# Kernel optimization log

Hardware: AMD Instinct MI355X
Metric: run time of the kernel (lower is better)

Reference implementation:

```python
import jax, jax.numpy as jnp
import numpy as np

# ---- problem constants (the torch module's `params` dict) ----
D = H = W = 128          # volume_shape
HS = WS = 128            # slice_shape
N_SLICES = 16
PSF = 3                  # PSF kernel is PSF^3 taps
K = PSF ** 3
RES_RATIO = 1.5          # res_s / res_r: slice pixel spacing in volume-voxel units
N_ITER = 10              # CG iterations (tol = 0.0 -> fixed trip count)
PSF_SIGMA = 0.8


def _corners(pts):
    """8-corner trilinear indices/weights with zero contribution out of bounds.
    pts: [..., 3] in (x, y, z) voxel coords. Returns (list of int32 linear idx, list of weights).
    Gather and scatter share this so A and At are exact transposes (required for CG)."""
    x, y, z = pts[..., 0], pts[..., 1], pts[..., 2]
    x0f, y0f, z0f = jnp.floor(x), jnp.floor(y), jnp.floor(z)
    fx, fy, fz = x - x0f, y - y0f, z - z0f
    x0, y0, z0 = x0f.astype(jnp.int32), y0f.astype(jnp.int32), z0f.astype(jnp.int32)
    idxs, ws = [], []
    for dz in (0, 1):
        for dy in (0, 1):
            for dx in (0, 1):
                xi, yi, zi = x0 + dx, y0 + dy, z0 + dz
                w = (fx if dx else 1.0 - fx) * (fy if dy else 1.0 - fy) * (fz if dz else 1.0 - fz)
                inb = (xi >= 0) & (xi < W) & (yi >= 0) & (yi < H) & (zi >= 0) & (zi < D)
                idxs.append(jnp.where(inb, (zi * H + yi) * W + xi, 0))
                ws.append(jnp.where(inb, w, 0.0))
    return idxs, ws


def _sample_points(transforms):
    """PSF sample points of every slice pixel mapped into volume voxel coords.
    transforms: [N, 3, 4] rigid (R | t). Returns [N, HS, WS, K, 3] in (x, y, z)."""
    u = (jnp.arange(WS, dtype=jnp.float32) - (WS - 1) / 2) * RES_RATIO
    v = (jnp.arange(HS, dtype=jnp.float32) - (HS - 1) / 2) * RES_RATIO
    base = jnp.stack(jnp.broadcast_arrays(u[None, :], v[:, None], jnp.zeros((HS, WS), jnp.float32)), -1)  # [HS,WS,3]
    ax = jnp.arange(PSF, dtype=jnp.float32) - (PSF - 1) / 2
    oz, oy, ox = jnp.meshgrid(ax, ax, ax, indexing='ij')
    offs = jnp.stack([ox.ravel(), oy.ravel(), oz.ravel()], -1)            # [K,3] voxel units
    pts = base[:, :, None, :] + offs[None, None, :, :]                     # [HS,WS,K,3] in slice frame
    R, t = transforms[:, :3, :3], transforms[:, :3, 3]
    pts = jnp.einsum('hwkc,nrc->nhwkr', pts, R) + t[:, None, None, None, :]
    center = jnp.array([(W - 1) / 2, (H - 1) / 2, (D - 1) / 2], jnp.float32)
    return pts + center


def A_op(transforms, vol, psf_flat):
    """slice_acquisition: PSF-weighted trilinear gather from volume -> slices [N,1,HS,WS]."""
    pts = _sample_points(transforms)
    flat = vol.reshape(-1)
    idxs, ws = _corners(pts)
    vals = sum(w * flat[i] for i, w in zip(idxs, ws))                      # [N,HS,WS,K]
    return jnp.einsum('nhwk,k->nhw', vals, psf_flat)[:, None]


def At_op(transforms, slices, psf_flat):
    """slice_acquisition_adjoint: PSF-weighted trilinear scatter-add of slices -> volume."""
    pts = _sample_points(transforms)
    wv = slices[:, 0, :, :, None] * psf_flat                               # [N,HS,WS,K]
    idxs, ws = _corners(pts)
    flat = jnp.zeros(D * H * W, slices.dtype)
    for i, w in zip(idxs, ws):
        flat = flat.at[i.reshape(-1)].add((w * wv).reshape(-1))
    return flat.reshape(1, 1, D, H, W)


def _dot(a, b):
    return jnp.vdot(a.reshape(-1), b.reshape(-1))


def cg_solve(AtA, b, x0, n_iter):
    r0 = b - AtA(x0)
    def body(state, _):
        x, r, p, rr = state
        Ap = AtA(p)
        alpha = rr / _dot(p, Ap)
        x = x + alpha * p
        r = r - alpha * Ap
        rr_new = _dot(r, r)
        p = r + (rr_new / rr) * p
        return (x, r, p, rr_new), None
    (x, _, _, _), _ = jax.lax.scan(body, (x0, r0, r0, _dot(r0, r0)), None, length=n_iter)
    return x


def _rigid_transforms(n, rng):
    # small random rotations (Rodrigues) + z-stacked translations, like motion-corrupted slice stacks
    ang = rng.uniform(-0.1, 0.1, (n, 3)).astype(np.float32)
    mats = []
    for a in ang:
        th = float(np.linalg.norm(a)) + 1e-8
        k = a / th
        Kx = np.array([[0, -k[2], k[1]], [k[2], 0, -k[0]], [-k[1], k[0], 0]], np.float32)
        mats.append(np.eye(3, dtype=np.float32) + np.sin(th) * Kx + (1 - np.cos(th)) * (Kx @ Kx))
    R = np.stack(mats)
    t = np.zeros((n, 3), np.float32)
    t[:, 2] = (np.arange(n) - (n - 1) / 2) * RES_RATIO
    t[:, :2] = rng.uniform(-2.0, 2.0, (n, 2)).astype(np.float32)
    return jnp.asarray(np.concatenate([R, t[:, :, None]], axis=-1))        # [n,3,4]


def setup_inputs() -> dict:
    key = jax.random.key(0)
    k1, k2 = jax.random.split(key)
    rng = np.random.default_rng(0)
    theta = _rigid_transforms(N_SLICES, rng)
    slices = jax.random.uniform(k1, (N_SLICES, 1, HS, WS), jnp.float32)
    volume = jax.random.uniform(k2, (1, 1, D, H, W), jnp.float32)
    ax = np.arange(PSF) - (PSF - 1) / 2
    zz, yy, xx = np.meshgrid(ax, ax, ax, indexing='ij')
    psf = np.exp(-(xx ** 2 + yy ** 2 + zz ** 2) / (2 * PSF_SIGMA ** 2)).astype(np.float32)
    psf /= psf.sum()
    return {"theta": theta, "slices": slices, "volume": volume, "psf": jnp.asarray(psf)}


def reference(theta, slices, volume, psf):
    psf_flat = psf.reshape(-1)
    AtA = lambda v: At_op(theta, A_op(theta, v, psf_flat), psf_flat)
    b = At_op(theta, slices, psf_flat)          # b = At(y); p is None, mu = 0
    x = cg_solve(AtA, b, volume, N_ITER)
    return jax.nn.relu(x)                       # output_relu=True
```

## Files before the change

### kernel.cpp

```cpp
#include <hip/hip_runtime.h>
#include <math.h>

constexpr int VOX = 128 * 128 * 128;
constexpr int NPIX = 16 * 128 * 128;
constexpr int NS = 16;
constexpr float RES_RATIO = 1.5f;
constexpr int CSTR = 128;
constexpr int TNX = 19, TNY = 19, TNZ = 10;


__global__ __launch_bounds__(512) void prep_kernel(
    const float* __restrict__ theta, const float* __restrict__ psf,
    float* __restrict__ cst, int* __restrict__ zb)
{
    int tid = threadIdx.x;
    int n = tid >> 5, j = tid & 31;
    if (n < NS) {
        const float* T = theta + n * 12;
        float* C = cst + n * CSTR;
        if (j < 12) C[j] = T[j];
        if (j == 12) {
            float r00=T[0], r01=T[1], r02=T[2],  t0=T[3];
            float r10=T[4], r11=T[5], r12=T[6],  t1=T[7];
            float r20=T[8], r21=T[9], r22=T[10], t2=T[11];
            float tc0 = t0 + 63.5f, tc1 = t1 + 63.5f, tc2 = t2 + 63.5f;
            C[12]=tc0; C[13]=tc1; C[14]=tc2;
            float C2 = fabsf(r02)+fabsf(r12)+fabsf(r22);
            C[15] = fabsf(r00)+fabsf(r10)+fabsf(r20);
            C[16] = fabsf(r01)+fabsf(r11)+fabsf(r21);
            C[17] = C2;
            C[18] = fabsf(r00)+fabsf(r01)+fabsf(r02);
            C[19] = fabsf(r10)+fabsf(r11)+fabsf(r12);
            C[20] = fabsf(r20)+fabsf(r21)+fabsf(r22);
            float mx = fmaxf(tc0, 127.0f - tc0);
            float my = fmaxf(tc1, 127.0f - tc1);
            float marg = 1.05f + C2 + fabsf(r02)*mx + fabsf(r12)*my;
            float inv = 1.0f / fabsf(r22);
            C[21] = tc2 - marg * inv;
            C[22] = tc2 + marg * inv;
        }
        if (j < 27) {
            float ox = (float)(j % 3) - 1.0f;
            float oy = (float)((j / 3) % 3) - 1.0f;
            float oz = (float)(j / 9) - 1.0f;
            C[24 + 3*j + 0] = T[0]*ox + T[1]*oy + T[2]*oz;
            C[24 + 3*j + 1] = T[4]*ox + T[5]*oy + T[6]*oz;
            C[24 + 3*j + 2] = T[8]*ox + T[9]*oy + T[10]*oz;
        }
    }
    __syncthreads();
    if (tid == 0) {
        float zmin = 1e30f, zmax = -1e30f;
        for (int s = 0; s < NS; ++s) {
            zmin = fminf(zmin, cst[s * CSTR + 21]);
            zmax = fmaxf(zmax, cst[s * CSTR + 22]);
        }
        zb[0] = max(0, (int)floorf(zmin));
        zb[1] = min(127, (int)ceilf(zmax));
        float* G = cst + NS * CSTR;
        float c = psf[13];
        float ic2 = 1.0f / (c * c);
        G[0]=psf[12]; G[1]=psf[13]; G[2]=psf[14];
        G[3]=psf[10]; G[4]=psf[13]; G[5]=psf[16];
        G[6]=psf[4]*ic2; G[7]=psf[13]*ic2; G[8]=psf[22]*ic2;
    }
}

__device__ __forceinline__ void block_reduce_spread(double s, double* slots)
{
    #pragma unroll
    for (int off = 32; off > 0; off >>= 1)
        s += __shfl_down(s, off, 64);
    __shared__ double ls[4];
    if ((threadIdx.x & 63) == 0) ls[threadIdx.x >> 6] = s;
    __syncthreads();
    if (threadIdx.x == 0)
        atomicAdd(&slots[(blockIdx.x & 63) * 32], ls[0] + ls[1] + ls[2] + ls[3]);
}

__device__ __forceinline__ void block_reduce3(
    double s0, double s1, double s2, double* a0, double* a1, double* a2)
{
    #pragma unroll
    for (int off = 32; off > 0; off >>= 1) {
        s0 += __shfl_down(s0, off, 64);
        s1 += __shfl_down(s1, off, 64);
        s2 += __shfl_down(s2, off, 64);
    }
    __shared__ double ls3[12];
    int wid = threadIdx.x >> 6;
    if ((threadIdx.x & 63) == 0) {
        ls3[wid*3+0] = s0; ls3[wid*3+1] = s1; ls3[wid*3+2] = s2;
    }
    __syncthreads();
    if (threadIdx.x == 0) {
        int sl = (blockIdx.x & 63) * 32;
        atomicAdd(&a0[sl], ls3[0]+ls3[3]+ls3[6]+ls3[9]);
        atomicAdd(&a1[sl], ls3[1]+ls3[4]+ls3[7]+ls3[10]);
        atomicAdd(&a2[sl], ls3[2]+ls3[5]+ls3[8]+ls3[11]);
    }
}

__global__ __launch_bounds__(64) void a_kernel(
    const float* __restrict__ cst, const float* __restrict__ vol,
    const float* __restrict__ psf, float* __restrict__ out,
    const float* __restrict__ subsrc,
    double* __restrict__ z1, double* __restrict__ z2, double* __restrict__ z3)
{
    int tid = threadIdx.x;
    if (blockIdx.x == 0) {
        for (int i = tid; i < 2048; i += 64) {
            if (z1) z1[i] = 0.0;
            if (z2) z2[i] = 0.0;
            if (z3) z3[i] = 0.0;
        }
    }

    int b = blockIdx.x;
    int n = b >> 8;
    int pb = b & 255;
    int w0 = (pb & 15) << 3, h0 = (pb >> 4) << 3;
    int w = w0 + (tid & 7), h = h0 + (tid >> 3);
    int oidx = (n << 14) + (h << 7) + w;
    float base = subsrc ? subsrc[oidx] : 0.0f;
    float sgn = subsrc ? -1.0f : 1.0f;

    const float* C = cst + n * CSTR;
    float r00=C[0], r01=C[1];
    float r10=C[4], r11=C[5];
    float r20=C[8], r21=C[9];

    float uc = (w0 + 3.5f - 63.5f) * RES_RATIO;
    float vc = (h0 + 3.5f - 63.5f) * RES_RATIO;
    const float du = 5.25f, dv = 5.25f;
    float cx = r00*uc + r01*vc + C[12];
    float cy = r10*uc + r11*vc + C[13];
    float cz = r20*uc + r21*vc + C[14];
    float hx = fabsf(r00)*du + fabsf(r01)*dv + C[18];
    float hy = fabsf(r10)*du + fabsf(r11)*dv + C[19];
    float hz = fabsf(r20)*du + fabsf(r21)*dv + C[20];
    int tx0 = (int)floorf(cx - hx);
    int ty0 = (int)floorf(cy - hy);
    int tz0 = (int)floorf(cz - hz);

    if (tx0 >= 128 || tx0 + TNX <= 0 || ty0 >= 128 || ty0 + TNY <= 0 ||
        tz0 >= 128 || tz0 + TNZ <= 0) {
        out[oidx] = base;
        return;
    }

    __shared__ float tile[TNZ * TNY * TNX];
    for (int i = tid; i < TNZ * TNY * TNX; i += 64) {
        int xx = i % TNX; int rem = i / TNX;
        int yy = rem % TNY; int zz = rem / TNY;
        int gx = tx0 + xx, gy = ty0 + yy, gz = tz0 + zz;
        bool ok = ((unsigned)gx < 128u) & ((unsigned)gy < 128u) & ((unsigned)gz < 128u);
        int off = ok ? ((gz << 14) + (gy << 7) + gx) : 0;
        float v = vol[off];
        tile[i] = ok ? v : 0.0f;
    }
    __syncthreads();

    float u = (w - 63.5f) * RES_RATIO;
    float v = (h - 63.5f) * RES_RATIO;
    float px = fmaf(r00, u, fmaf(r01, v, C[12])) - (float)tx0;
    float py = fmaf(r10, u, fmaf(r11, v, C[13])) - (float)ty0;
    float pz = fmaf(r20, u, fmaf(r21, v, C[14])) - (float)tz0;

    const float* O = C + 24;
    float acc = 0.0f;
    for (int k = 0; k < 27; ++k) {
        float sx = px + O[3*k+0];
        float sy = py + O[3*k+1];
        float sz = pz + O[3*k+2];
        int x0 = (int)sx, y0 = (int)sy, z0 = (int)sz;
        float fx = sx - (float)x0, fy = sy - (float)y0, fz = sz - (float)z0;
        const float* tp = tile + (z0 * TNY + y0) * TNX + x0;
        float c000 = tp[0],             c001 = tp[1];
        float c010 = tp[TNX],           c011 = tp[TNX+1];
        float c100 = tp[TNY*TNX],       c101 = tp[TNY*TNX+1];
        float c110 = tp[TNY*TNX+TNX],   c111 = tp[TNY*TNX+TNX+1];
        float c00 = fmaf(fx, c001 - c000, c000);
        float c01 = fmaf(fx, c011 - c010, c010);
        float c10 = fmaf(fx, c101 - c100, c100);
        float c11 = fmaf(fx, c111 - c110, c110);
        float c0  = fmaf(fy, c01 - c00, c00);
        float c1  = fmaf(fy, c11 - c10, c10);
        acc = fmaf(psf[k], fmaf(fz, c1 - c0, c0), acc);
    }
    out[oidx] = fmaf(sgn, acc, base);
}

__global__ __launch_bounds__(256) void at_scatter_kernel(
    const float* __restrict__ cst, const float* __restrict__ sl,
    float* __restrict__ outvol)
{
    int id = blockIdx.x * 256 + threadIdx.x;
    int x = id & 127, y = (id >> 7) & 127, n = id >> 14;
    const float* C = cst + n * CSTR;
    float r00=C[0], r01=C[1], r02=C[2];
    float r10=C[4], r11=C[5], r12=C[6];
    float r20=C[8], r21=C[9], r22=C[10];
    float tc2 = C[14];
    float C0=C[15], C1=C[16], C2=C[17];

    float gx = (float)x - C[12];
    float gy = (float)y - C[13];

    float az = r02*gx + r12*gy - r22*tc2;
    float lim = 1.0f + C2 + 0.01f;
    float inv22 = 1.0f / r22;
    int z0 = (int)ceilf((-lim - az) * inv22);
    int z1v = (int)floorf(( lim - az) * inv22);
    z0 = max(z0, 0); z1v = min(z1v, 127);
    if (z0 > z1v) return;

    float ax = r00*gx + r10*gy - r20*tc2;
    float ay = r01*gx + r11*gy - r21*tc2;

    float gpxa = fmaf(r20, (float)z0, ax), gpxb = fmaf(r20, (float)z1v, ax);
    float gpya = fmaf(r21, (float)z0, ay), gpyb = fmaf(r21, (float)z1v, ay);
    int m2a = (int)floorf(2.0f*(gpxa + 95.25f - C0)) + 601;
    int m2b = (int)floorf(2.0f*(gpxb + 95.25f - C0)) + 601;
    int n2a = (int)floorf(2.0f*(gpya + 95.25f - C1)) + 601;
    int n2b = (int)floorf(2.0f*(gpyb + 95.25f - C1)) + 601;
    int wb0 = min(m2a, m2b) / 3;
    int hb0 = min(n2a, n2b) / 3;

    const float* slice_n = sl + (n << 14);
    float s[4][4];
    #pragma unroll
    for (int aa = 0; aa < 4; ++aa) {
        int hv = hb0 - 200 + aa;
        bool hok = ((unsigned)hv < 128u);
        #pragma unroll
        for (int cc = 0; cc < 4; ++cc) {
            int wv = wb0 - 200 + cc;
            bool ok = hok & ((unsigned)wv < 128u);
            int off = ok ? ((hv << 7) + wv) : 0;
            float vs = slice_n[off];
            s[aa][cc] = ok ? vs : 0.0f;
        }
    }

    const float* G = cst + NS * CSTR;
    float pfx0=G[0], pfx1=G[1], pfx2=G[2];
    float pfy0=G[3], pfy1=G[4], pfy2=G[5];
    float pfz0=G[6], pfz1=G[7], pfz2=G[8];

    int yx = (y << 7) + x;

    for (int z = z0; z <= z1v; ++z) {
        float fzv = (float)z;
        float gpx = fmaf(r20, fzv, ax);
        float gpy = fmaf(r21, fzv, ay);
        float gz  = fzv - tc2;
        int m2 = (int)floorf(2.0f*(gpx + 95.25f - C0)) + 601;
        int n2 = (int)floorf(2.0f*(gpy + 95.25f - C1)) + 601;

        float fxv[5], cA[5], cB[5], cC[5], cD[5], Axa[5], Aya[5], Aza[5];
        #pragma unroll
        for (int i = 0; i < 5; ++i) {
            int m = m2 + i;
            int ki = m - (m / 3) * 3;
            int twoj = (ki == 0) ? 0 : ((ki == 1) ? -2 : 2);
            int wi = (m - twoj) / 3;
            int ci = wi - wb0;
            fxv[i] = (ki == 0) ? pfx1 : ((ki == 1) ? pfx0 : pfx2);
            cA[i] = (ci==0)?s[0][0]:((ci==1)?s[0][1]:((ci==2)?s[0][2]:s[0][3]));
            cB[i] = (ci==0)?s[1][0]:((ci==1)?s[1][1]:((ci==2)?s[1][2]:s[1][3]));
            cC[i] = (ci==0)?s[2][0]:((ci==1)?s[2][1]:((ci==2)?s[2][2]:s[2][3]));
            cD[i] = (ci==0)?s[3][0]:((ci==1)?s[3][1]:((ci==2)?s[3][2]:s[3][3]));
            float mu = 0.5f * (float)(m - 600) - 95.25f;
            Axa[i] = fmaf(r00, mu, -gx);
            Aya[i] = fmaf(r10, mu, -gy);
            Aza[i] = fmaf(r20, mu, -gz);
        }
        float fyv[5], mvv[5];
        int rj[5];
        #pragma unroll
        for (int j = 0; j < 5; ++j) {
            int m = n2 + j;
            int kj = m - (m / 3) * 3;
            int twoj = (kj == 0) ? 0 : ((kj == 1) ? -2 : 2);
            int hj = (m - twoj) / 3;
            rj[j] = hj - hb0;
            fyv[j] = (kj == 0) ? pfy1 : ((kj == 1) ? pfy0 : pfy2);
            mvv[j] = 0.5f * (float)(m - 600) - 95.25f;
        }

        float acc0 = 0.0f, acc1 = 0.0f;
        #pragma unroll
        for (int i = 0; i < 5; ++i) {
            #pragma unroll
            for (int j = 0; j < 5; ++j) {
                float sval = (rj[j]==0) ? cA[i]
                           : ((rj[j]==1) ? cB[i]
                           : ((rj[j]==2) ? cC[i] : cD[i]));
                float svf = sval * fxv[i] * fyv[j];
                float Bx = fmaf(r01, mvv[j], Axa[i]);
                float By = fmaf(r11, mvv[j], Aya[i]);
                float Bz = fmaf(r21, mvv[j], Aza[i]);
                float w0 = fmaxf(1.0f - fabsf(Bx - r02), 0.0f)
                         * fmaxf(1.0f - fabsf(By - r12), 0.0f)
                         * fmaxf(1.0f - fabsf(Bz - r22), 0.0f);
                float w1 = fmaxf(1.0f - fabsf(Bx), 0.0f)
                         * fmaxf(1.0f - fabsf(By), 0.0f)
                         * fmaxf(1.0f - fabsf(Bz), 0.0f);
                float w2 = fmaxf(1.0f - fabsf(Bx + r02), 0.0f)
                         * fmaxf(1.0f - fabsf(By + r12), 0.0f)
                         * fmaxf(1.0f - fabsf(Bz + r22), 0.0f);
                float t = fmaf(w0, pfz0, fmaf(w1, pfz1, w2 * pfz2));
                if (i & 1) acc1 = fmaf(t, svf, acc1);
                else       acc0 = fmaf(t, svf, acc0);
            }
        }
        atomicAdd(&outvol[(z << 14) + yx], acc0 + acc1);
    }
}

__global__ __launch_bounds__(256) void initpr_kernel(
    const float* __restrict__ r, float* __restrict__ p, float* __restrict__ Ap,
    double* __restrict__ rr_slots, const int* __restrict__ zb)
{
    int z = blockIdx.x >> 6;
    if (z < zb[0] || z > zb[1]) return;
    int i = blockIdx.x * 256 + threadIdx.x;
    float rv = r[i];
    p[i] = rv;
    Ap[i] = 0.0f;
    block_reduce_spread((double)rv * (double)rv, rr_slots);
}

__global__ __launch_bounds__(256) void dots_kernel(
    const float* __restrict__ Ap, const float* __restrict__ p,
    const float* __restrict__ r,
    double* __restrict__ s_pap, double* __restrict__ s_rap,
    double* __restrict__ s_apap, const int* __restrict__ zb)
{
    int z = blockIdx.x >> 6;
    if (z < zb[0] || z > zb[1]) return;
    int i = blockIdx.x * 256 + threadIdx.x;
    double a = (double)Ap[i];
    block_reduce3(a * (double)p[i], a * (double)r[i], a * a,
                  s_pap, s_rap, s_apap);
}

__global__ __launch_bounds__(256) void update_kernel(
    float* __restrict__ x, float* __restrict__ r, float* __restrict__ p,
    float* __restrict__ Ap,
    const double* __restrict__ rr_src, int rr_is_slots,
    const double* __restrict__ paps, const double* __restrict__ raps,
    const double* __restrict__ apaps, double* __restrict__ rr_out,
    const int* __restrict__ zb, float* __restrict__ outp)
{
    __shared__ float sh_ab[2];
    int tid = threadIdx.x;
    if (tid < 64) {
        double v0 = rr_is_slots ? rr_src[tid * 32] : 0.0;
        double v1 = paps[tid * 32];
        double v2 = raps[tid * 32];
        double v3 = apaps[tid * 32];
        #pragma unroll
        for (int off = 32; off > 0; off >>= 1) {
            v0 += __shfl_down(v0, off, 64);
            v1 += __shfl_down(v1, off, 64);
            v2 += __shfl_down(v2, off, 64);
            v3 += __shfl_down(v3, off, 64);
        }
        if (tid == 0) {
            double rr_old = rr_is_slots ? v0 : rr_src[0];
            double alpha = rr_old / v1;
            double rr_new = rr_old - 2.0 * alpha * v2 + alpha * alpha * v3;
            if (blockIdx.x == 0) rr_out[0] = rr_new;
            sh_ab[0] = (float)alpha;
            sh_ab[1] = (float)(rr_new / rr_old);
        }
    }
    __syncthreads();
    float af = sh_ab[0], bf = sh_ab[1];

    int z = blockIdx.x >> 6;
    int i = blockIdx.x * 256 + tid;
    bool inslab = (z >= zb[0]) & (z <= zb[1]);
    if (!inslab) {
        if (outp) outp[i] = fmaxf(x[i], 0.0f);
        return;
    }
    float xv = fmaf(af, p[i], x[i]);
    x[i] = xv;
    float apv = Ap[i];
    Ap[i] = 0.0f;
    float rvv = fmaf(-af, apv, r[i]);
    r[i] = rvv;
    p[i] = fmaf(bf, p[i], rvv);
    if (outp) outp[i] = fmaxf(xv, 0.0f);
}

extern "C" void kernel_launch(void* const* d_in, const int* in_sizes, int n_in,
                              void* d_out, int out_size, void* d_ws, size_t ws_size,
                              hipStream_t stream) {
    const float* theta  = (const float*)d_in[0];
    const float* slices = (const float*)d_in[1];
    const float* volume = (const float*)d_in[2];
    const float* psf    = (const float*)d_in[3];
    float* out = (float*)d_out;

    char* ws = (char*)d_ws;
    float* x  = (float*)ws;
    float* r  = x  + VOX;
    float* p  = r  + VOX;
    float* Ap = p  + VOX;
    float* sl = Ap + VOX;
    double* sc = (double*)(sl + NPIX);
    double* rrs0  = sc;
    double* paps  = sc + 2048;
    double* raps  = sc + 4096;
    double* apaps = sc + 6144;
    double* rr_sc = sc + 8192;
    float* cst = (float*)(sc + 8208);
    int* zb = (int*)(cst + NS * CSTR + 16);

    const int gapix = NPIX / 64;
    const int gvox = VOX / 256;
    const int gsc  = NPIX / 256;

    prep_kernel<<<1, 512, 0, stream>>>(theta, psf, cst, zb);

    hipMemcpyAsync(x, volume, VOX * sizeof(float), hipMemcpyDeviceToDevice, stream);
    hipMemsetAsync(r, 0, 2 * VOX * sizeof(float), stream);

    a_kernel<<<gapix, 64, 0, stream>>>(cst, x, psf, sl, slices, rrs0, nullptr, nullptr);
    at_scatter_kernel<<<gsc, 256, 0, stream>>>(cst, sl, r);
    initpr_kernel<<<gvox, 256, 0, stream>>>(r, p, Ap, rrs0, zb);

    for (int it = 0; it < 10; ++it) {
        a_kernel<<<gapix, 64, 0, stream>>>(cst, p, psf, sl, nullptr, paps, raps, apaps);
        at_scatter_kernel<<<gsc, 256, 0, stream>>>(cst, sl, Ap);
        dots_kernel<<<gvox, 256, 0, stream>>>(Ap, p, r, paps, raps, apaps, zb);

        const double* rr_src = (it == 0) ? rrs0 : &rr_sc[it];
        update_kernel<<<gvox, 256, 0, stream>>>(
            x, r, p, Ap, rr_src, (it == 0) ? 1 : 0,
            paps, raps, apaps, &rr_sc[it + 1], zb, (it == 9) ? out : nullptr);
    }
}
```

Baseline: 991.4 us.

## Parallelize at_scatter over z by giving each thread one z-plane

New measurement: 955.0 us. 1.04x faster.

```diff
diff --git a/kernel.cpp b/kernel.cpp
--- a/kernel.cpp
+++ b/kernel.cpp
@@ -7,6 +7,7 @@
 constexpr float RES_RATIO = 1.5f;
 constexpr int CSTR = 128;
 constexpr int TNX = 19, TNY = 19, TNZ = 10;
+constexpr int ZSL = 5;
 
 
 __global__ __launch_bounds__(512) void prep_kernel(
@@ -196,7 +197,8 @@
     float* __restrict__ outvol)
 {
     int id = blockIdx.x * 256 + threadIdx.x;
-    int x = id & 127, y = (id >> 7) & 127, n = id >> 14;
+    int x = id & 127, y = (id >> 7) & 127;
+    int n = (id >> 14) & 15, zi = id >> 18;
     const float* C = cst + n * CSTR;
     float r00=C[0], r01=C[1], r02=C[2];
     float r10=C[4], r11=C[5], r12=C[6];
@@ -213,28 +215,29 @@
     int z0 = (int)ceilf((-lim - az) * inv22);
     int z1v = (int)floorf(( lim - az) * inv22);
     z0 = max(z0, 0); z1v = min(z1v, 127);
-    if (z0 > z1v) return;
+    int z = z0 + zi;
+    if (z > z1v) return;
 
     float ax = r00*gx + r10*gy - r20*tc2;
     float ay = r01*gx + r11*gy - r21*tc2;
 
-    float gpxa = fmaf(r20, (float)z0, ax), gpxb = fmaf(r20, (float)z1v, ax);
-    float gpya = fmaf(r21, (float)z0, ay), gpyb = fmaf(r21, (float)z1v, ay);
-    int m2a = (int)floorf(2.0f*(gpxa + 95.25f - C0)) + 601;
-    int m2b = (int)floorf(2.0f*(gpxb + 95.25f - C0)) + 601;
-    int n2a = (int)floorf(2.0f*(gpya + 95.25f - C1)) + 601;
-    int n2b = (int)floorf(2.0f*(gpyb + 95.25f - C1)) + 601;
-    int wb0 = min(m2a, m2b) / 3;
-    int hb0 = min(n2a, n2b) / 3;
+    float fzv = (float)z;
+    float gpx = fmaf(r20, fzv, ax);
+    float gpy = fmaf(r21, fzv, ay);
+    float gz  = fzv - tc2;
+    int m2 = (int)floorf(2.0f*(gpx + 95.25f - C0)) + 601;
+    int n2 = (int)floorf(2.0f*(gpy + 95.25f - C1)) + 601;
+    int wb0 = m2 / 3;
+    int hb0 = n2 / 3;
 
     const float* slice_n = sl + (n << 14);
-    float s[4][4];
-    #pragma unroll
-    for (int aa = 0; aa < 4; ++aa) {
+    float s[3][3];
+    #pragma unroll
+    for (int aa = 0; aa < 3; ++aa) {
         int hv = hb0 - 200 + aa;
         bool hok = ((unsigned)hv < 128u);
         #pragma unroll
-        for (int cc = 0; cc < 4; ++cc) {
+        for (int cc = 0; cc < 3; ++cc) {
             int wv = wb0 - 200 + cc;
             bool ok = hok & ((unsigned)wv < 128u);
             int off = ok ? ((hv << 7) + wv) : 0;
@@ -250,73 +253,62 @@
 
     int yx = (y << 7) + x;
 
-    for (int z = z0; z <= z1v; ++z) {
-        float fzv = (float)z;
-        float gpx = fmaf(r20, fzv, ax);
-        float gpy = fmaf(r21, fzv, ay);
-        float gz  = fzv - tc2;
-        int m2 = (int)floorf(2.0f*(gpx + 95.25f - C0)) + 601;
-        int n2 = (int)floorf(2.0f*(gpy + 95.25f - C1)) + 601;
-
-        float fxv[5], cA[5], cB[5], cC[5], cD[5], Axa[5], Aya[5], Aza[5];
-        #pragma unroll
-        for (int i = 0; i < 5; ++i) {
-            int m = m2 + i;
-            int ki = m - (m / 3) * 3;
-            int twoj = (ki == 0) ? 0 : ((ki == 1) ? -2 : 2);
-            int wi = (m - twoj) / 3;
-            int ci = wi - wb0;
-            fxv[i] = (ki == 0) ? pfx1 : ((ki == 1) ? pfx0 : pfx2);
-            cA[i] = (ci==0)?s[0][0]:((ci==1)?s[0][1]:((ci==2)?s[0][2]:s[0][3]));
-            cB[i] = (ci==0)?s[1][0]:((ci==1)?s[1][1]:((ci==2)?s[1][2]:s[1][3]));
-            cC[i] = (ci==0)?s[2][0]:((ci==1)?s[2][1]:((ci==2)?s[2][2]:s[2][3]));
-            cD[i] = (ci==0)?s[3][0]:((ci==1)?s[3][1]:((ci==2)?s[3][2]:s[3][3]));
-            float mu = 0.5f * (float)(m - 600) - 95.25f;
-            Axa[i] = fmaf(r00, mu, -gx);
-            Aya[i] = fmaf(r10, mu, -gy);
-            Aza[i] = fmaf(r20, mu, -gz);
-        }
-        float fyv[5], mvv[5];
-        int rj[5];
+    float fxv[5], cA[5], cB[5], cC[5], Axa[5], Aya[5], Aza[5];
+    #pragma unroll
+    for (int i = 0; i < 5; ++i) {
+        int m = m2 + i;
+        int ki = m - (m / 3) * 3;
+        int twoj = (ki == 0) ? 0 : ((ki == 1) ? -2 : 2);
+        int wi = (m - twoj) / 3;
+        int ci = wi - wb0;
+        fxv[i] = (ki == 0) ? pfx1 : ((ki == 1) ? pfx0 : pfx2);
+        cA[i] = (ci==0)?s[0][0]:((ci==1)?s[0][1]:s[0][2]);
+        cB[i] = (ci==0)?s[1][0]:((ci==1)?s[1][1]:s[1][2]);
+        cC[i] = (ci==0)?s[2][0]:((ci==1)?s[2][1]:s[2][2]);
+        float mu = 0.5f * (float)(m - 600) - 95.25f;
+        Axa[i] = fmaf(r00, mu, -gx);
+        Aya[i] = fmaf(r10, mu, -gy);
+        Aza[i] = fmaf(r20, mu, -gz);
+    }
+    float fyv[5], mvv[5];
+    int rj[5];
+    #pragma unroll
+    for (int j = 0; j < 5; ++j) {
+        int m = n2 + j;
+        int kj = m - (m / 3) * 3;
+        int twoj = (kj == 0) ? 0 : ((kj == 1) ? -2 : 2);
+        int hj = (m - twoj) / 3;
+        rj[j] = hj - hb0;
+        fyv[j] = (kj == 0) ? pfy1 : ((kj == 1) ? pfy0 : pfy2);
+        mvv[j] = 0.5f * (float)(m - 600) - 95.25f;
+    }
+
+    float acc0 = 0.0f, acc1 = 0.0f;
+    #pragma unroll
+    for (int i = 0; i < 5; ++i) {
         #pragma unroll
         for (int j = 0; j < 5; ++j) {
-            int m = n2 + j;
-            int kj = m - (m / 3) * 3;
-            int twoj = (kj == 0) ? 0 : ((kj == 1) ? -2 : 2);
-            int hj = (m - twoj) / 3;
-            rj[j] = hj - hb0;
-            fyv[j] = (kj == 0) ? pfy1 : ((kj == 1) ? pfy0 : pfy2);
-            mvv[j] = 0.5f * (float)(m - 600) - 95.25f;
-        }
-
-        float acc0 = 0.0f, acc1 = 0.0f;
-        #pragma unroll
-        for (int i = 0; i < 5; ++i) {
-            #pragma unroll
-            for (int j = 0; j < 5; ++j) {
-                float sval = (rj[j]==0) ? cA[i]
-                           : ((rj[j]==1) ? cB[i]
-                           : ((rj[j]==2) ? cC[i] : cD[i]));
-                float svf = sval * fxv[i] * fyv[j];
-                float Bx = fmaf(r01, mvv[j], Axa[i]);
-                float By = fmaf(r11, mvv[j], Aya[i]);
-                float Bz = fmaf(r21, mvv[j], Aza[i]);
-                float w0 = fmaxf(1.0f - fabsf(Bx - r02), 0.0f)
-                         * fmaxf(1.0f - fabsf(By - r12), 0.0f)
-                         * fmaxf(1.0f - fabsf(Bz - r22), 0.0f);
-                float w1 = fmaxf(1.0f - fabsf(Bx), 0.0f)
-                         * fmaxf(1.0f - fabsf(By), 0.0f)
-                         * fmaxf(1.0f - fabsf(Bz), 0.0f);
-                float w2 = fmaxf(1.0f - fabsf(Bx + r02), 0.0f)
-                         * fmaxf(1.0f - fabsf(By + r12), 0.0f)
-                         * fmaxf(1.0f - fabsf(Bz + r22), 0.0f);
-                float t = fmaf(w0, pfz0, fmaf(w1, pfz1, w2 * pfz2));
-                if (i & 1) acc1 = fmaf(t, svf, acc1);
-                else       acc0 = fmaf(t, svf, acc0);
-            }
-        }
-        atomicAdd(&outvol[(z << 14) + yx], acc0 + acc1);
-    }
+            float sval = (rj[j]==0) ? cA[i]
+                       : ((rj[j]==1) ? cB[i] : cC[i]);
+            float svf = sval * fxv[i] * fyv[j];
+            float Bx = fmaf(r01, mvv[j], Axa[i]);
+            float By = fmaf(r11, mvv[j], Aya[i]);
+            float Bz = fmaf(r21, mvv[j], Aza[i]);
+            float w0 = fmaxf(1.0f - fabsf(Bx - r02), 0.0f)
+                     * fmaxf(1.0f - fabsf(By - r12), 0.0f)
+                     * fmaxf(1.0f - fabsf(Bz - r22), 0.0f);
+            float w1 = fmaxf(1.0f - fabsf(Bx), 0.0f)
+                     * fmaxf(1.0f - fabsf(By), 0.0f)
+                     * fmaxf(1.0f - fabsf(Bz), 0.0f);
+            float w2 = fmaxf(1.0f - fabsf(Bx + r02), 0.0f)
+                     * fmaxf(1.0f - fabsf(By + r12), 0.0f)
+                     * fmaxf(1.0f - fabsf(Bz + r22), 0.0f);
+            float t = fmaf(w0, pfz0, fmaf(w1, pfz1, w2 * pfz2));
+            if (i & 1) acc1 = fmaf(t, svf, acc1);
+            else       acc0 = fmaf(t, svf, acc0);
+        }
+    }
+    atomicAdd(&outvol[(z << 14) + yx], acc0 + acc1);
 }
 
 __global__ __launch_bounds__(256) void initpr_kernel(
@@ -423,7 +415,7 @@
 
     const int gapix = NPIX / 64;
     const int gvox = VOX / 256;
-    const int gsc  = NPIX / 256;
+    const int gsc  = NPIX * ZSL / 256;
 
     prep_kernel<<<1, 512, 0, stream>>>(theta, psf, cst, zb);
 
```
